# Performance work log

Hardware: AMD Instinct MI355X
Metric: run time of the kernel (lower is better)

## Reference

```python
import jax, jax.numpy as jnp
import numpy as np

E = 8          # n_experts
TOP_K = 2      # n_active_experts


def setup_inputs() -> dict:
    key = jax.random.key(0)
    ks = jax.random.split(key, 9)
    B, S, D, H = 4, 2048, 2048, 1408
    w = 0.02  # weight scale for numerical stability
    return {
        "x": jax.random.normal(ks[0], (B, S, D), dtype=jnp.float32),
        "gate_w": jax.random.normal(ks[1], (E, D), dtype=jnp.float32) * w,
        "expert_bias": jnp.zeros((E,), dtype=jnp.float32),
        "Wg": jax.random.normal(ks[2], (E, H, D), dtype=jnp.float32) * w,
        "Wu": jax.random.normal(ks[3], (E, H, D), dtype=jnp.float32) * w,
        "Wd": jax.random.normal(ks[4], (E, D, H), dtype=jnp.float32) * w,
        "Ws_g": jax.random.normal(ks[5], (H, D), dtype=jnp.float32) * w,
        "Ws_u": jax.random.normal(ks[6], (H, D), dtype=jnp.float32) * w,
        "Ws_d": jax.random.normal(ks[7], (D, H), dtype=jnp.float32) * w,
    }


def _swiglu(x, wg, wu, wd):
    # torch Linear layout: y = x @ W.T
    return (jax.nn.silu(x @ wg.T) * (x @ wu.T)) @ wd.T


def reference(x, gate_w, expert_bias, Wg, Wu, Wd, Ws_g, Ws_u, Ws_d):
    B, S, D = x.shape
    flat = x.reshape(-1, D)                      # [N, D]
    N = flat.shape[0]

    logits = flat @ gate_w.T                     # [N, E]
    probs = jax.nn.softmax(logits, axis=-1)
    biased = logits + expert_bias
    _, top_idx = jax.lax.top_k(biased, TOP_K)    # [N, K] (bias used only for selection)
    top_w = jnp.take_along_axis(probs, top_idx, axis=-1)
    top_w = top_w / jnp.sum(top_w, axis=-1, keepdims=True)

    # dense per-token combine weights: cw[n, e] = sum_k top_w[n,k] * (top_idx[n,k]==e)
    rows = jnp.arange(N)[:, None]
    cw = jnp.zeros((N, E), dtype=flat.dtype).at[rows, top_idx].add(top_w)

    out = jnp.zeros_like(flat)
    for e in range(E):  # fixed small expert count; equivalent to gather/scatter dispatch
        out = out + cw[:, e:e + 1] * _swiglu(flat, Wg[e], Wu[e], Wd[e])

    out = out + _swiglu(flat, Ws_g, Ws_u, Ws_d)  # shared expert
    return out.reshape(B, S, D)
```

## Files before the change

### kernel.cpp

```cpp
#include <hip/hip_runtime.h>
#include <hip/hip_bf16.h>

#define N_TOK 8192
#define DDIM  2048
#define HDIM  1408
#define ROWS_R 16384
#define ROWS_T 24576
#define MAXTILES 104
#define BM 256
#define BN 128
#define BK 64

typedef unsigned short u16;
typedef unsigned int   u32;
typedef __bf16 bf16x8 __attribute__((ext_vector_type(8)));
typedef float  f32x4  __attribute__((ext_vector_type(4)));

__device__ __forceinline__ u16 f2bf(float f) {
  union { float f; u32 u; } v; v.f = f;
  u32 u = v.u;
  return (u16)((u + 0x7fffu + ((u >> 16) & 1u)) >> 16);
}
__device__ __forceinline__ float bf2f(u16 b) {
  union { u32 u; float f; } v; v.u = ((u32)b) << 16; return v.f;
}

typedef __attribute__((address_space(1))) void gvoid;
typedef __attribute__((address_space(3))) void lvoid;
__device__ __forceinline__ void gload16(const void* g, void* l) {
  __builtin_amdgcn_global_load_lds((gvoid*)g, (lvoid*)l, 16, 0, 0);
}

#define BAR __builtin_amdgcn_s_barrier()
#define SP1 __builtin_amdgcn_s_setprio(1)
#define SP0 __builtin_amdgcn_s_setprio(0)
#define LGK0 do { asm volatile("s_waitcnt lgkmcnt(0)" ::: "memory"); \
                  __builtin_amdgcn_sched_barrier(0); } while (0)
#define VMCNT(n) asm volatile("s_waitcnt vmcnt(" #n ")" ::: "memory")

#define READ_AF(base, mb, dst) { \
  _Pragma("unroll") for (int m_ = 0; m_ < 2; ++m_) { \
    int r_ = ((mb) >> 1) * 128 + wr * 32 + m_ * 16 + l15; \
    _Pragma("unroll") for (int kk_ = 0; kk_ < 2; ++kk_) { \
      int cch_ = kk_ * 4 + lhi; \
      (dst)[m_ * 2 + kk_] = *(const bf16x8*)((const char*)(base) + r_ * 128 + ((cch_ ^ (r_ & 7)) * 16)); } } }

#define READ_BF(base, dst) { \
  _Pragma("unroll") for (int n_ = 0; n_ < 4; ++n_) { \
    int r_ = wc * 64 + n_ * 16 + l15; \
    _Pragma("unroll") for (int kk_ = 0; kk_ < 2; ++kk_) { \
      int cch_ = kk_ * 4 + lhi; \
      (dst)[n_ * 2 + kk_] = *(const bf16x8*)((const char*)(base) + r_ * 128 + ((cch_ ^ (r_ & 7)) * 16)); } } }

#define MFMAQ(AF, BB, ACC, MB) { \
  _Pragma("unroll") for (int m_ = 0; m_ < 2; ++m_) \
  _Pragma("unroll") for (int n_ = 0; n_ < 4; ++n_) \
  _Pragma("unroll") for (int kk_ = 0; kk_ < 2; ++kk_) \
    (ACC)[(MB) + m_][n_] = __builtin_amdgcn_mfma_f32_16x16x32_bf16((AF)[m_ * 2 + kk_], (BB)[n_ * 2 + kk_], (ACC)[(MB) + m_][n_], 0, 0, 0); }

__global__ void k_gate(const float* __restrict__ x, const float* __restrict__ gw,
                       const float* __restrict__ bias, int* __restrict__ tok_idx,
                       float* __restrict__ wts, int* __restrict__ counts,
                       u16* __restrict__ xb) {
  int lane = threadIdx.x & 63;
  int n = blockIdx.x * 4 + (threadIdx.x >> 6);
  const float* xr = x + (size_t)n * DDIM;
  u16* xbr = xb + (size_t)n * DDIM;
  float acc[8];
#pragma unroll
  for (int e = 0; e < 8; ++e) acc[e] = 0.f;
#pragma unroll 2
  for (int j0 = 0; j0 < DDIM; j0 += 256) {
    float4 xv = *(const float4*)(xr + j0 + lane * 4);
    u32 p0 = (u32)f2bf(xv.x) | ((u32)f2bf(xv.y) << 16);
    u32 p1 = (u32)f2bf(xv.z) | ((u32)f2bf(xv.w) << 16);
    *(uint2*)(xbr + j0 + lane * 4) = make_uint2(p0, p1);
#pragma unroll
    for (int e = 0; e < 8; ++e) {
      float4 gv = *(const float4*)(gw + e * DDIM + j0 + lane * 4);
      acc[e] += xv.x * gv.x + xv.y * gv.y + xv.z * gv.z + xv.w * gv.w;
    }
  }
#pragma unroll
  for (int e = 0; e < 8; ++e) {
#pragma unroll
    for (int off = 32; off > 0; off >>= 1) acc[e] += __shfl_xor(acc[e], off);
  }
  if (lane == 0) {
    float m = acc[0];
    for (int e = 1; e < 8; ++e) m = fmaxf(m, acc[e]);
    float p[8];
    for (int e = 0; e < 8; ++e) p[e] = expf(acc[e] - m);
    float b0[8];
    for (int e = 0; e < 8; ++e) b0[e] = acc[e] + bias[e];
    int i0 = 0;
    for (int e = 1; e < 8; ++e) if (b0[e] > b0[i0]) i0 = e;
    int i1 = (i0 == 0) ? 1 : 0;
    for (int e = 0; e < 8; ++e) if (e != i0 && b0[e] > b0[i1]) i1 = e;
    float w0 = p[i0], w1 = p[i1], inv = 1.f / (w0 + w1);
    tok_idx[2 * n] = i0; tok_idx[2 * n + 1] = i1;
    wts[2 * n] = w0 * inv; wts[2 * n + 1] = w1 * inv;
    atomicAdd(&counts[i0], 1); atomicAdd(&counts[i1], 1);
  }
}

__global__ void k_scan(const int* __restrict__ counts, int* __restrict__ offsets,
                       int* __restrict__ cursors, int* __restrict__ ntiles,
                       int4* __restrict__ tiles) {
  if (threadIdx.x != 0 || blockIdx.x != 0) return;
  int off = 0, idx = 0;
  for (int e = 0; e < 8; ++e) {
    offsets[e] = off; cursors[e] = 0;
    int T = counts[e];
    for (int r = 0; r < T; r += BM) {
      int nr = T - r; if (nr > BM) nr = BM;
      tiles[idx++] = make_int4(e, off + r, nr, 0);
    }
    off += T;
  }
  offsets[8] = off;
  for (int r = 0; r < N_TOK; r += BM)
    tiles[idx++] = make_int4(8, ROWS_R + r, BM, 0);
  *ntiles = idx;
}

__global__ void k_build(const int* __restrict__ tok_idx, const int* __restrict__ offsets,
                        int* __restrict__ cursors, int* __restrict__ token_ids,
                        int* __restrict__ pos) {
  int n = blockIdx.x * blockDim.x + threadIdx.x;
  if (n >= N_TOK) return;
#pragma unroll
  for (int s = 0; s < 2; ++s) {
    int e = tok_idx[2 * n + s];
    int p = offsets[e] + atomicAdd(&cursors[e], 1);
    token_ids[p] = n;
    pos[2 * n + s] = p;
  }
  token_ids[ROWS_R + n] = n;
}

__global__ void k_convall(const float* __restrict__ Wg, const float* __restrict__ Wsg,
                          const float* __restrict__ Wu, const float* __restrict__ Wsu,
                          const float* __restrict__ Wd, const float* __restrict__ Wsd,
                          u16* __restrict__ wgb, u16* __restrict__ wub, u16* __restrict__ wdb) {
  const long PER = (long)9 * HDIM * DDIM / 8;
  const long BIG = (long)8 * HDIM * DDIM / 8;
  const long TOT = 3 * PER;
  long stride = (long)gridDim.x * blockDim.x;
  for (long i = (long)blockIdx.x * blockDim.x + threadIdx.x; i < TOT; i += stride) {
    int g = (int)(i / PER);
    long r = i - (long)g * PER;
    const float* src; u16* dst;
    if (g == 0)      { dst = wgb; src = (r < BIG) ? Wg + r * 8 : Wsg + (r - BIG) * 8; }
    else if (g == 1) { dst = wub; src = (r < BIG) ? Wu + r * 8 : Wsu + (r - BIG) * 8; }
    else             { dst = wdb; src = (r < BIG) ? Wd + r * 8 : Wsd + (r - BIG) * 8; }
    float4 a = ((const float4*)src)[0], b = ((const float4*)src)[1];
    u32 p0 = (u32)f2bf(a.x) | ((u32)f2bf(a.y) << 16);
    u32 p1 = (u32)f2bf(a.z) | ((u32)f2bf(a.w) << 16);
    u32 p2 = (u32)f2bf(b.x) | ((u32)f2bf(b.y) << 16);
    u32 p3 = (u32)f2bf(b.z) | ((u32)f2bf(b.w) << 16);
    ((uint4*)dst)[r] = make_uint4(p0, p1, p2, p3);
  }
}

__global__ __launch_bounds__(512, 2) void k_gemm1(
    const u16* __restrict__ xb, const u16* __restrict__ wgb,
    const int* __restrict__ token_ids, const int* __restrict__ ntiles,
    const int4* __restrict__ tiles, u16* __restrict__ h) {
  __shared__ u16 As[2][BM * BK];
  __shared__ u16 Bgs[2][BN * BK];
  __shared__ u16 Bus[2][BN * BK];

  int ntl = *ntiles;
  int nwg = (HDIM / BN) * ntl;
  int bid = blockIdx.x;
  if (bid >= nwg) return;
  int q8 = nwg >> 3, r8 = nwg & 7;
  int xcd = bid & 7, pp = bid >> 3;
  int lid = (xcd < r8 ? xcd * (q8 + 1) : r8 * (q8 + 1) + (xcd - r8) * q8) + pp;
  int bx = lid / ntl, tile = lid - bx * ntl;

  int4 tl = tiles[tile];
  int set = tl.x, grow = tl.y, nrows = tl.z;

  int t = threadIdx.x;
  int wid = t >> 6, lane = t & 63;
  int wr = wid >> 1, wc = wid & 1;
  int l15 = lane & 15, lhi = lane >> 4;

  const u16* aptr[4];
#pragma unroll
  for (int i = 0; i < 4; ++i) {
    int chunk = i * 512 + t;
    int r = chunk >> 3, cc = chunk & 7;
    int c = cc ^ (r & 7);
    int rr = r < nrows ? r : nrows - 1;
    int tok = token_ids[grow + rr];
    aptr[i] = xb + (size_t)tok * DDIM + c * 8;
  }
  const u16* gptr[2];
#pragma unroll
  for (int i = 0; i < 2; ++i) {
    int chunk = i * 512 + t;
    int r = chunk >> 3, cc = chunk & 7;
    int c = cc ^ (r & 7);
    gptr[i] = wgb + (size_t)set * (HDIM * DDIM) + (size_t)(bx * BN + r) * DDIM + c * 8;
  }
  const size_t WUOFF = (size_t)9 * HDIM * DDIM;

#define G1_A0(b, k0) { gload16(aptr[0] + (k0), (char*)As[b] + (size_t)t * 16); \
                       gload16(aptr[1] + (k0), (char*)As[b] + (size_t)(512 + t) * 16); }
#define G1_A1(b, k0) { gload16(aptr[2] + (k0), (char*)As[b] + (size_t)(1024 + t) * 16); \
                       gload16(aptr[3] + (k0), (char*)As[b] + (size_t)(1536 + t) * 16); }
#define G1_BG(b, k0) { gload16(gptr[0] + (k0), (char*)Bgs[b] + (size_t)t * 16); \
                       gload16(gptr[1] + (k0), (char*)Bgs[b] + (size_t)(512 + t) * 16); }
#define G1_BU(b, k0) { gload16(gptr[0] + WUOFF + (k0), (char*)Bus[b] + (size_t)t * 16); \
                       gload16(gptr[1] + WUOFF + (k0), (char*)Bus[b] + (size_t)(512 + t) * 16); }

  f32x4 accg[4][4], accu[4][4];
  f32x4 z = {0.f, 0.f, 0.f, 0.f};
#pragma unroll
  for (int m = 0; m < 4; ++m)
#pragma unroll
    for (int n = 0; n < 4; ++n) { accg[m][n] = z; accu[m][n] = z; }

  const int NK = DDIM / BK;

  VMCNT(0);
  G1_BG(0, 0); G1_A0(0, 0); G1_A1(0, 0); G1_BU(0, 0);
  VMCNT(4); BAR;

  for (int kt = 0; kt < NK - 1; ++kt) {
    int cur = kt & 1, nxt = cur ^ 1;
    int k1 = (kt + 1) * BK;
    bf16x8 a01[4], a23[4], bb[8];
    READ_AF(As[cur], 0, a01);
    READ_BF(Bgs[cur], bb);
    G1_BG(nxt, k1);
    BAR; LGK0;
    SP1; MFMAQ(a01, bb, accg, 0); SP0;
    VMCNT(4); BAR;
    READ_AF(As[cur], 2, a23);
    G1_A0(nxt, k1);
    BAR; LGK0;
    SP1; MFMAQ(a23, bb, accg, 2); SP0;
    VMCNT(4); BAR;
    READ_BF(Bus[cur], bb);
    G1_A1(nxt, k1);
    BAR; LGK0;
    SP1; MFMAQ(a01, bb, accu, 0); SP0;
    BAR;
    G1_BU(nxt, k1);
    BAR;
    SP1; MFMAQ(a23, bb, accu, 2); SP0;
    VMCNT(4); BAR;
  }
  {
    int cur = (NK - 1) & 1;
    VMCNT(0); BAR;
    bf16x8 a01[4], a23[4], bg8[8], bu8[8];
    READ_AF(As[cur], 0, a01);
    READ_AF(As[cur], 2, a23);
    READ_BF(Bgs[cur], bg8);
    READ_BF(Bus[cur], bu8);
    LGK0;
    MFMAQ(a01, bg8, accg, 0); MFMAQ(a23, bg8, accg, 2);
    MFMAQ(a01, bu8, accu, 0); MFMAQ(a23, bu8, accu, 2);
  }

#pragma unroll
  for (int m = 0; m < 4; ++m) {
#pragma unroll
    for (int n = 0; n < 4; ++n) {
      int col = bx * BN + wc * 64 + n * 16 + l15;
#pragma unroll
      for (int qq = 0; qq < 4; ++qq) {
        int rl = (m >> 1) * 128 + wr * 32 + (m & 1) * 16 + lhi * 4 + qq;
        if (rl < nrows) {
          float g = accg[m][n][qq], u = accu[m][n][qq];
          float hv = g / (1.f + expf(-g)) * u;
          h[(size_t)(grow + rl) * HDIM + col] = f2bf(hv);
        }
      }
    }
  }
#undef G1_A0
#undef G1_A1
#undef G1_BG
#undef G1_BU
}

__global__ __launch_bounds__(512, 2) void k_gemm2(
    const u16* __restrict__ h, const u16* __restrict__ wdb,
    const int* __restrict__ ntiles, const int4* __restrict__ tiles,
    u16* __restrict__ y) {
  __shared__ u16 As2[3][BM * BK];
  __shared__ u16 Bs2[3][BN * BK];

  int ntl = *ntiles;
  int nwg = (DDIM / BN) * ntl;
  int bid = blockIdx.x;
  if (bid >= nwg) return;
  int q8 = nwg >> 3, r8 = nwg & 7;
  int xcd = bid & 7, pp = bid >> 3;
  int lid = (xcd < r8 ? xcd * (q8 + 1) : r8 * (q8 + 1) + (xcd - r8) * q8) + pp;
  int bx = lid / ntl, tile = lid - bx * ntl;

  int4 tl = tiles[tile];
  int set = tl.x, grow = tl.y, nrows = tl.z;

  int t = threadIdx.x;
  int wid = t >> 6, lane = t & 63;
  int wr = wid >> 1, wc = wid & 1;
  int l15 = lane & 15, lhi = lane >> 4;

  const u16* aptr[4];
#pragma unroll
  for (int i = 0; i < 4; ++i) {
    int chunk = i * 512 + t;
    int r = chunk >> 3, cc = chunk & 7;
    int c = cc ^ (r & 7);
    aptr[i] = h + (size_t)(grow + r) * HDIM + c * 8;
  }
  const u16* bptr[2];
#pragma unroll
  for (int i = 0; i < 2; ++i) {
    int chunk = i * 512 + t;
    int r = chunk >> 3, cc = chunk & 7;
    int c = cc ^ (r & 7);
    bptr[i] = wdb + (size_t)set * (DDIM * HDIM) + (size_t)(bx * BN + r) * HDIM + c * 8;
  }

#define G2_A(b, k0) { gload16(aptr[0] + (k0), (char*)As2[b] + (size_t)t * 16); \
                      gload16(aptr[1] + (k0), (char*)As2[b] + (size_t)(512 + t) * 16); \
                      gload16(aptr[2] + (k0), (char*)As2[b] + (size_t)(1024 + t) * 16); \
                      gload16(aptr[3] + (k0), (char*)As2[b] + (size_t)(1536 + t) * 16); }
#define G2_B(b, k0) { gload16(bptr[0] + (k0), (char*)Bs2[b] + (size_t)t * 16); \
                      gload16(bptr[1] + (k0), (char*)Bs2[b] + (size_t)(512 + t) * 16); }

  f32x4 acc[4][4];
  f32x4 z = {0.f, 0.f, 0.f, 0.f};
#pragma unroll
  for (int m = 0; m < 4; ++m)
#pragma unroll
    for (int n = 0; n < 4; ++n) acc[m][n] = z;

  const int NK2 = HDIM / BK;

  VMCNT(0);
  G2_A(0, 0); G2_B(0, 0);
  G2_A(1, BK); G2_B(1, BK);
  VMCNT(6); BAR;

  for (int kt = 0; kt < NK2 - 2; ++kt) {
    int cur = kt % 3, nx2 = (kt + 2) % 3;
    int k2 = (kt + 2) * BK;
    bf16x8 a01[4], a23[4], bb[8];
    READ_AF(As2[cur], 0, a01);
    READ_BF(Bs2[cur], bb);
    G2_A(nx2, k2);
    BAR; LGK0;
    SP1; MFMAQ(a01, bb, acc, 0); SP0;
    BAR;
    READ_AF(As2[cur], 2, a23);
    G2_B(nx2, k2);
    BAR; LGK0;
    SP1; MFMAQ(a23, bb, acc, 2); SP0;
    VMCNT(6); BAR;
  }
  VMCNT(0); BAR;
  for (int kt = NK2 - 2; kt < NK2; ++kt) {
    int cur = kt % 3;
    bf16x8 a01[4], a23[4], bb[8];
    READ_AF(As2[cur], 0, a01);
    READ_AF(As2[cur], 2, a23);
    READ_BF(Bs2[cur], bb);
    LGK0;
    MFMAQ(a01, bb, acc, 0); MFMAQ(a23, bb, acc, 2);
  }

#pragma unroll
  for (int m = 0; m < 4; ++m) {
#pragma unroll
    for (int n = 0; n < 4; ++n) {
      int col = bx * BN + wc * 64 + n * 16 + l15;
#pragma unroll
      for (int qq = 0; qq < 4; ++qq) {
        int rl = (m >> 1) * 128 + wr * 32 + (m & 1) * 16 + lhi * 4 + qq;
        if (rl < nrows)
          y[(size_t)(grow + rl) * DDIM + col] = f2bf(acc[m][n][qq]);
      }
    }
  }
#undef G2_A
#undef G2_B
}

__global__ void k_comb(const u16* __restrict__ y, const int* __restrict__ pos,
                       const float* __restrict__ wts, float* __restrict__ out) {
  int n = blockIdx.x;
  int c8 = threadIdx.x;
  int p0 = pos[2 * n], p1 = pos[2 * n + 1];
  float w0 = wts[2 * n], w1 = wts[2 * n + 1];
  uint4 a = ((const uint4*)(y + (size_t)p0 * DDIM))[c8];
  uint4 b = ((const uint4*)(y + (size_t)p1 * DDIM))[c8];
  uint4 c = ((const uint4*)(y + (size_t)(ROWS_R + n) * DDIM))[c8];
  float* o = out + (size_t)n * DDIM + c8 * 8;
#pragma unroll
  for (int j = 0; j < 4; ++j) {
    u32 ua = ((const u32*)&a)[j], ub = ((const u32*)&b)[j], uc = ((const u32*)&c)[j];
    o[2 * j]     = w0 * bf2f((u16)(ua & 0xffff)) + w1 * bf2f((u16)(ub & 0xffff)) + bf2f((u16)(uc & 0xffff));
    o[2 * j + 1] = w0 * bf2f((u16)(ua >> 16))    + w1 * bf2f((u16)(ub >> 16))    + bf2f((u16)(uc >> 16));
  }
}

extern "C" void kernel_launch(void* const* d_in, const int* in_sizes, int n_in,
                              void* d_out, int out_size, void* d_ws, size_t ws_size,
                              hipStream_t stream) {
  const float* x    = (const float*)d_in[0];
  const float* gw   = (const float*)d_in[1];
  const float* bias = (const float*)d_in[2];
  const float* Wg   = (const float*)d_in[3];
  const float* Wu   = (const float*)d_in[4];
  const float* Wd   = (const float*)d_in[5];
  const float* Wsg  = (const float*)d_in[6];
  const float* Wsu  = (const float*)d_in[7];
  const float* Wsd  = (const float*)d_in[8];
  float* out = (float*)d_out;

  char* ws = (char*)d_ws;
  size_t off = 0;
  auto alloc = [&](size_t bytes) -> void* {
    void* p = ws + off;
    off += (bytes + 255) & ~(size_t)255;
    return p;
  };
  u16* xb  = (u16*)alloc((size_t)N_TOK * DDIM * 2);
  u16* wgb = (u16*)alloc((size_t)9 * HDIM * DDIM * 2);
  u16* wub = (u16*)alloc((size_t)9 * HDIM * DDIM * 2);
  u16* wdb = (u16*)alloc((size_t)9 * DDIM * HDIM * 2);
  u16* h   = (u16*)alloc((size_t)ROWS_T * HDIM * 2);
  u16* y   = (u16*)alloc((size_t)ROWS_T * DDIM * 2);
  int*   token_ids = (int*)alloc(ROWS_T * 4);
  int*   tok_idx   = (int*)alloc(N_TOK * 2 * 4);
  int*   pos       = (int*)alloc(N_TOK * 2 * 4);
  float* wts       = (float*)alloc(N_TOK * 2 * 4);
  int*   counts  = (int*)alloc(8 * 4);
  int*   offsets = (int*)alloc(9 * 4);
  int*   cursors = (int*)alloc(8 * 4);
  int*   ntiles  = (int*)alloc(4);
  int4*  tiles   = (int4*)alloc(MAXTILES * 16);

  hipMemsetAsync(counts, 0, 8 * 4, stream);
  k_gate<<<N_TOK / 4, 256, 0, stream>>>(x, gw, bias, tok_idx, wts, counts, xb);
  k_scan<<<1, 64, 0, stream>>>(counts, offsets, cursors, ntiles, tiles);
  k_build<<<(N_TOK + 255) / 256, 256, 0, stream>>>(tok_idx, offsets, cursors, token_ids, pos);

  k_convall<<<4096, 256, 0, stream>>>(Wg, Wsg, Wu, Wsu, Wd, Wsd, wgb, wub, wdb);

  k_gemm1<<<(HDIM / BN) * MAXTILES, 512, 0, stream>>>(xb, wgb, token_ids, ntiles, tiles, h);
  k_gemm2<<<(DDIM / BN) * MAXTILES, 512, 0, stream>>>(h, wdb, ntiles, tiles, y);
  k_comb<<<N_TOK, 256, 0, stream>>>(y, pos, wts, out);
}
```

Baseline: 963.5 us.

## Widen gemm2 tile to 256 columns with two B halves and double buffering

The down-projection GEMM now computes a 256x256 output tile per workgroup. It uses two 128-column B halves and two accumulator sets, replacing the 128-column triple-buffered version, so each A tile loaded from h is reused across twice as many output columns. The gemm1 schedule is also reordered to load A before B, and the per-wave row mapping is changed to contiguous 64-row blocks. The cost is more accumulator registers and fewer workgroups, which could hurt occupancy or load balance.

```diff
diff --git a/kernel.cpp b/kernel.cpp
--- a/kernel.cpp
+++ b/kernel.cpp
@@ -40,7 +40,7 @@
 
 #define READ_AF(base, mb, dst) { \
   _Pragma("unroll") for (int m_ = 0; m_ < 2; ++m_) { \
-    int r_ = ((mb) >> 1) * 128 + wr * 32 + m_ * 16 + l15; \
+    int r_ = wr * 64 + ((mb) + m_) * 16 + l15; \
     _Pragma("unroll") for (int kk_ = 0; kk_ < 2; ++kk_) { \
       int cch_ = kk_ * 4 + lhi; \
       (dst)[m_ * 2 + kk_] = *(const bf16x8*)((const char*)(base) + r_ * 128 + ((cch_ ^ (r_ & 7)) * 16)); } } }
@@ -227,8 +227,8 @@
   const int NK = DDIM / BK;
 
   VMCNT(0);
-  G1_BG(0, 0); G1_A0(0, 0); G1_A1(0, 0); G1_BU(0, 0);
-  VMCNT(4); BAR;
+  G1_A0(0, 0); G1_A1(0, 0); G1_BG(0, 0); G1_BU(0, 0);
+  VMCNT(2); BAR;
 
   for (int kt = 0; kt < NK - 1; ++kt) {
     int cur = kt & 1, nxt = cur ^ 1;
@@ -236,24 +236,24 @@
     bf16x8 a01[4], a23[4], bb[8];
     READ_AF(As[cur], 0, a01);
     READ_BF(Bgs[cur], bb);
-    G1_BG(nxt, k1);
+    G1_A0(nxt, k1);
     BAR; LGK0;
     SP1; MFMAQ(a01, bb, accg, 0); SP0;
-    VMCNT(4); BAR;
+    BAR;
     READ_AF(As[cur], 2, a23);
-    G1_A0(nxt, k1);
+    G1_A1(nxt, k1);
     BAR; LGK0;
     SP1; MFMAQ(a23, bb, accg, 2); SP0;
     VMCNT(4); BAR;
     READ_BF(Bus[cur], bb);
-    G1_A1(nxt, k1);
+    G1_BG(nxt, k1);
     BAR; LGK0;
     SP1; MFMAQ(a01, bb, accu, 0); SP0;
     BAR;
     G1_BU(nxt, k1);
     BAR;
     SP1; MFMAQ(a23, bb, accu, 2); SP0;
-    VMCNT(4); BAR;
+    VMCNT(2); BAR;
   }
   {
     int cur = (NK - 1) & 1;
@@ -275,7 +275,7 @@
       int col = bx * BN + wc * 64 + n * 16 + l15;
 #pragma unroll
       for (int qq = 0; qq < 4; ++qq) {
-        int rl = (m >> 1) * 128 + wr * 32 + (m & 1) * 16 + lhi * 4 + qq;
+        int rl = wr * 64 + m * 16 + lhi * 4 + qq;
         if (rl < nrows) {
           float g = accg[m][n][qq], u = accu[m][n][qq];
           float hv = g / (1.f + expf(-g)) * u;
@@ -294,11 +294,12 @@
     const u16* __restrict__ h, const u16* __restrict__ wdb,
     const int* __restrict__ ntiles, const int4* __restrict__ tiles,
     u16* __restrict__ y) {
-  __shared__ u16 As2[3][BM * BK];
-  __shared__ u16 Bs2[3][BN * BK];
+  __shared__ u16 As[2][BM * BK];
+  __shared__ u16 B0s[2][BN * BK];
+  __shared__ u16 B1s[2][BN * BK];
 
   int ntl = *ntiles;
-  int nwg = (DDIM / BN) * ntl;
+  int nwg = (DDIM / 256) * ntl;
   int bid = blockIdx.x;
   if (bid >= nwg) return;
   int q8 = nwg >> 3, r8 = nwg & 7;
@@ -322,78 +323,95 @@
     int c = cc ^ (r & 7);
     aptr[i] = h + (size_t)(grow + r) * HDIM + c * 8;
   }
-  const u16* bptr[2];
-#pragma unroll
-  for (int i = 0; i < 2; ++i) {
+  const u16* bptr[4];
+#pragma unroll
+  for (int i = 0; i < 4; ++i) {
     int chunk = i * 512 + t;
     int r = chunk >> 3, cc = chunk & 7;
     int c = cc ^ (r & 7);
-    bptr[i] = wdb + (size_t)set * (DDIM * HDIM) + (size_t)(bx * BN + r) * HDIM + c * 8;
-  }
-
-#define G2_A(b, k0) { gload16(aptr[0] + (k0), (char*)As2[b] + (size_t)t * 16); \
-                      gload16(aptr[1] + (k0), (char*)As2[b] + (size_t)(512 + t) * 16); \
-                      gload16(aptr[2] + (k0), (char*)As2[b] + (size_t)(1024 + t) * 16); \
-                      gload16(aptr[3] + (k0), (char*)As2[b] + (size_t)(1536 + t) * 16); }
-#define G2_B(b, k0) { gload16(bptr[0] + (k0), (char*)Bs2[b] + (size_t)t * 16); \
-                      gload16(bptr[1] + (k0), (char*)Bs2[b] + (size_t)(512 + t) * 16); }
-
-  f32x4 acc[4][4];
+    bptr[i] = wdb + (size_t)set * (DDIM * HDIM) + (size_t)(bx * 256 + r) * HDIM + c * 8;
+  }
+
+#define G2_A0(b, k0) { gload16(aptr[0] + (k0), (char*)As[b] + (size_t)t * 16); \
+                       gload16(aptr[1] + (k0), (char*)As[b] + (size_t)(512 + t) * 16); }
+#define G2_A1(b, k0) { gload16(aptr[2] + (k0), (char*)As[b] + (size_t)(1024 + t) * 16); \
+                       gload16(aptr[3] + (k0), (char*)As[b] + (size_t)(1536 + t) * 16); }
+#define G2_B0(b, k0) { gload16(bptr[0] + (k0), (char*)B0s[b] + (size_t)t * 16); \
+                       gload16(bptr[1] + (k0), (char*)B0s[b] + (size_t)(512 + t) * 16); }
+#define G2_B1(b, k0) { gload16(bptr[2] + (k0), (char*)B1s[b] + (size_t)t * 16); \
+                       gload16(bptr[3] + (k0), (char*)B1s[b] + (size_t)(512 + t) * 16); }
+
+  f32x4 acc0[4][4], acc1[4][4];
   f32x4 z = {0.f, 0.f, 0.f, 0.f};
 #pragma unroll
   for (int m = 0; m < 4; ++m)
 #pragma unroll
-    for (int n = 0; n < 4; ++n) acc[m][n] = z;
-
-  const int NK2 = HDIM / BK;
+    for (int n = 0; n < 4; ++n) { acc0[m][n] = z; acc1[m][n] = z; }
+
+  const int NK = HDIM / BK;
 
   VMCNT(0);
-  G2_A(0, 0); G2_B(0, 0);
-  G2_A(1, BK); G2_B(1, BK);
-  VMCNT(6); BAR;
-
-  for (int kt = 0; kt < NK2 - 2; ++kt) {
-    int cur = kt % 3, nx2 = (kt + 2) % 3;
-    int k2 = (kt + 2) * BK;
+  G2_A0(0, 0); G2_A1(0, 0); G2_B0(0, 0); G2_B1(0, 0);
+  VMCNT(2); BAR;
+
+  for (int kt = 0; kt < NK - 1; ++kt) {
+    int cur = kt & 1, nxt = cur ^ 1;
+    int k1 = (kt + 1) * BK;
     bf16x8 a01[4], a23[4], bb[8];
-    READ_AF(As2[cur], 0, a01);
-    READ_BF(Bs2[cur], bb);
-    G2_A(nx2, k2);
-    BAR; LGK0;
-    SP1; MFMAQ(a01, bb, acc, 0); SP0;
-    BAR;
-    READ_AF(As2[cur], 2, a23);
-    G2_B(nx2, k2);
-    BAR; LGK0;
-    SP1; MFMAQ(a23, bb, acc, 2); SP0;
-    VMCNT(6); BAR;
-  }
-  VMCNT(0); BAR;
-  for (int kt = NK2 - 2; kt < NK2; ++kt) {
-    int cur = kt % 3;
-    bf16x8 a01[4], a23[4], bb[8];
-    READ_AF(As2[cur], 0, a01);
-    READ_AF(As2[cur], 2, a23);
-    READ_BF(Bs2[cur], bb);
+    READ_AF(As[cur], 0, a01);
+    READ_BF(B0s[cur], bb);
+    G2_A0(nxt, k1);
+    BAR; LGK0;
+    SP1; MFMAQ(a01, bb, acc0, 0); SP0;
+    BAR;
+    READ_AF(As[cur], 2, a23);
+    G2_A1(nxt, k1);
+    BAR; LGK0;
+    SP1; MFMAQ(a23, bb, acc0, 2); SP0;
+    VMCNT(4); BAR;
+    READ_BF(B1s[cur], bb);
+    G2_B0(nxt, k1);
+    BAR; LGK0;
+    SP1; MFMAQ(a01, bb, acc1, 0); SP0;
+    BAR;
+    G2_B1(nxt, k1);
+    BAR;
+    SP1; MFMAQ(a23, bb, acc1, 2); SP0;
+    VMCNT(2); BAR;
+  }
+  {
+    int cur = (NK - 1) & 1;
+    VMCNT(0); BAR;
+    bf16x8 a01[4], a23[4], b08[8], b18[8];
+    READ_AF(As[cur], 0, a01);
+    READ_AF(As[cur], 2, a23);
+    READ_BF(B0s[cur], b08);
+    READ_BF(B1s[cur], b18);
     LGK0;
-    MFMAQ(a01, bb, acc, 0); MFMAQ(a23, bb, acc, 2);
+    MFMAQ(a01, b08, acc0, 0); MFMAQ(a23, b08, acc0, 2);
+    MFMAQ(a01, b18, acc1, 0); MFMAQ(a23, b18, acc1, 2);
   }
 
 #pragma unroll
   for (int m = 0; m < 4; ++m) {
 #pragma unroll
     for (int n = 0; n < 4; ++n) {
-      int col = bx * BN + wc * 64 + n * 16 + l15;
+      int col = bx * 256 + wc * 64 + n * 16 + l15;
 #pragma unroll
       for (int qq = 0; qq < 4; ++qq) {
-        int rl = (m >> 1) * 128 + wr * 32 + (m & 1) * 16 + lhi * 4 + qq;
-        if (rl < nrows)
-          y[(size_t)(grow + rl) * DDIM + col] = f2bf(acc[m][n][qq]);
+        int rl = wr * 64 + m * 16 + lhi * 4 + qq;
+        if (rl < nrows) {
+          size_t rowoff = (size_t)(grow + rl) * DDIM;
+          y[rowoff + col]       = f2bf(acc0[m][n][qq]);
+          y[rowoff + col + 128] = f2bf(acc1[m][n][qq]);
+        }
       }
     }
   }
-#undef G2_A
-#undef G2_B
+#undef G2_A0
+#undef G2_A1
+#undef G2_B0
+#undef G2_B1
 }
 
 __global__ void k_comb(const u16* __restrict__ y, const int* __restrict__ pos,
@@ -459,6 +477,6 @@
   k_convall<<<4096, 256, 0, stream>>>(Wg, Wsg, Wu, Wsu, Wd, Wsd, wgb, wub, wdb);
 
   k_gemm1<<<(HDIM / BN) * MAXTILES, 512, 0, stream>>>(xb, wgb, token_ids, ntiles, tiles, h);
-  k_gemm2<<<(DDIM / BN) * MAXTILES, 512, 0, stream>>>(h, wdb, ntiles, tiles, y);
+  k_gemm2<<<(DDIM / 256) * MAXTILES, 512, 0, stream>>>(h, wdb, ntiles, tiles, y);
   k_comb<<<N_TOK, 256, 0, stream>>>(y, pos, wts, out);
 }
```

Result: faster. 873.8 us (-9.3%).
